# Kernel optimization log

Measured on AMD Instinct MI355X. Metric: run time of the kernel, lower is better.

Reference implementation:

```python
import jax, jax.numpy as jnp
import numpy as np
import math

B, L, E, H, K = 4, 1024, 1024, 16, 64
D = E // H  # head_dim = 64; rel_pe has 2K+1 = 129 rows


def setup_inputs() -> dict:
    key = jax.random.key(0)
    ks = jax.random.split(key, 4)
    s = 1.0 / math.sqrt(E)
    return {
        "q": jax.random.normal(ks[0], (B, L, E), dtype=jnp.float32),
        "in_proj_weight": jax.random.normal(ks[1], (3 * E, E), dtype=jnp.float32) * s,
        "in_proj_bias": jnp.zeros((3 * E,), dtype=jnp.float32),
        "out_w": jax.random.normal(ks[2], (E, E), dtype=jnp.float32) * s,
        "out_b": jnp.zeros((E,), dtype=jnp.float32),
        "rel_pe": jax.random.normal(ks[3], (2 * K + 1, D), dtype=jnp.float32) * (1.0 / math.sqrt(D)),
    }


def _attend(q, in_proj_weight, in_proj_bias, out_w, out_b, rel_pe):
    b, l, e = q.shape
    h, d = H, D
    qkv = q @ in_proj_weight.T + in_proj_bias  # (B, L, 3E)
    qh, kh, vh = jnp.split(qkv, 3, axis=-1)
    # (B, L, E) -> (B, H, L, D)
    qh = qh.reshape(b, l, h, d).transpose(0, 2, 1, 3)
    kh = kh.reshape(b, l, h, d).transpose(0, 2, 1, 3)
    vh = vh.reshape(b, l, h, d).transpose(0, 2, 1, 3)
    qh = qh / math.sqrt(d)  # scaling applies to both content and position terms
    # content scores
    scores = jnp.einsum("bhid,bhjd->bhij", qh, kh)
    # relative-position bias: a[i, j] = rel_pe[clip(j - i, -K, K) + K]
    # compute q . rel_pe once, then gather per (i, j) -- same math as the
    # original O(L^2 * D) materialized tensor, without building it.
    pos = jnp.arange(l)
    rel = jnp.clip(pos[None, :] - pos[:, None], -K, K) + K  # (L, L) int
    bias_r = jnp.einsum("bhid,rd->bhir", qh, rel_pe)  # (B, H, L, 2K+1)
    bias = jnp.take_along_axis(bias_r, jnp.broadcast_to(rel[None, None], (b, h, l, l)), axis=-1)
    attn = jax.nn.softmax(scores + bias, axis=-1)
    out = jnp.einsum("bhij,bhjd->bhid", attn, vh)  # (B, H, L, D)
    out = out.transpose(0, 2, 1, 3).reshape(b, l, e)
    return out @ out_w.T + out_b


def reference(q, in_proj_weight, in_proj_bias, out_w, out_b, rel_pe):
    return _attend(q, in_proj_weight, in_proj_bias, out_w, out_b, rel_pe)
```

## Files before the change

### kernel.cpp

```cpp
#include <hip/hip_runtime.h>
#include <math.h>

typedef _Float16 half_t;
typedef _Float16 half8 __attribute__((ext_vector_type(8)));
typedef _Float16 half4v __attribute__((ext_vector_type(4)));
typedef float float4v __attribute__((ext_vector_type(4)));
typedef float float16v __attribute__((ext_vector_type(16)));

#define AS1 __attribute__((address_space(1)))
#define AS3 __attribute__((address_space(3)))

#define MFMA16(a, b, c) __builtin_amdgcn_mfma_f32_16x16x32_f16((a), (b), (c), 0, 0, 0)
#define MFMA32(a, b, c) __builtin_amdgcn_mfma_f32_32x32x16_f16((a), (b), (c), 0, 0, 0)

__device__ __forceinline__ void gload16(const half_t* g, half_t* l) {
    __builtin_amdgcn_global_load_lds((const AS1 void*)g, (AS3 void*)l, 16, 0, 0);
}

__device__ __forceinline__ int iclamp(int v, int lo, int hi) {
    return v < lo ? lo : (v > hi ? hi : v);
}

__global__ __launch_bounds__(256) void cast_kernel(
    const float* __restrict__ q, const float* __restrict__ w_in,
    const float* __restrict__ w_out, const float* __restrict__ pe,
    half_t* __restrict__ q16, half_t* __restrict__ w16,
    half_t* __restrict__ wo16, half_t* __restrict__ pe16)
{
    const int tid = blockIdx.x * 256 + threadIdx.x;
    const int stride = gridDim.x * 256;
    for (int i = tid; i < 1048576; i += stride) {
        float4 v = ((const float4*)q)[i];
        *(half4v*)(q16 + (size_t)i * 4) =
            (half4v){(half_t)v.x, (half_t)v.y, (half_t)v.z, (half_t)v.w};
    }
    for (int i = tid; i < 786432; i += stride) {
        float4 v = ((const float4*)w_in)[i];
        *(half4v*)(w16 + (size_t)i * 4) =
            (half4v){(half_t)v.x, (half_t)v.y, (half_t)v.z, (half_t)v.w};
    }
    for (int i = tid; i < 262144; i += stride) {
        float4 v = ((const float4*)w_out)[i];
        *(half4v*)(wo16 + (size_t)i * 4) =
            (half4v){(half_t)v.x, (half_t)v.y, (half_t)v.z, (half_t)v.w};
    }
    for (int i = tid; i < 2064; i += stride) {
        float4 v = ((const float4*)pe)[i];
        *(half4v*)(pe16 + (size_t)i * 4) =
            (half4v){(half_t)v.x, (half_t)v.y, (half_t)v.z, (half_t)v.w};
    }
    for (int i = tid; i < 496; i += stride) {
        *(half4v*)(pe16 + 8256 + (size_t)i * 4) = (half4v){0, 0, 0, 0};
    }
}

__global__ __launch_bounds__(256) void qkv_gemm(
    const half_t* __restrict__ A, const half_t* __restrict__ W,
    const float* __restrict__ bias,
    half_t* __restrict__ qh, half_t* __restrict__ kh, half_t* __restrict__ vt)
{
    __shared__ half_t As[128 * 32];
    __shared__ half_t Bs[128 * 32];
    const int K = 1024;
    const int tid = threadIdx.x, lane = tid & 63, wid = tid >> 6;
    const int wm = wid & 1, wn = wid >> 1;
    const int bid = blockIdx.x;
    const int xcd = bid & 7, idx = bid >> 3;
    const int m0 = (((xcd >> 1) << 3) + (idx & 7)) * 128;
    const int n0 = (((xcd & 1) * 12) + (idx >> 3)) * 128;

    const half_t* gA[2]; const half_t* gB[2];
    half_t* lA[2]; half_t* lB[2];
    {
        const int base = wid * 128;
#pragma unroll
        for (int c = 0; c < 2; ++c) {
            int slot = base + c * 64 + lane;
            int row = slot >> 2;
            int ch = (slot & 3) ^ ((row >> 1) & 3);
            gA[c] = A + (size_t)(m0 + row) * K + ch * 8;
            gB[c] = W + (size_t)(n0 + row) * K + ch * 8;
            lA[c] = As + (base + c * 64) * 8;
            lB[c] = Bs + (base + c * 64) * 8;
        }
    }
    int aOff[4], bOff[4];
#pragma unroll
    for (int i = 0; i < 4; ++i) {
        int ra = wm * 64 + i * 16 + (lane & 15);
        aOff[i] = ra * 32 + (((lane >> 4) ^ ((ra >> 1) & 3)) * 8);
        int rb = wn * 64 + i * 16 + (lane & 15);
        bOff[i] = rb * 32 + (((lane >> 4) ^ ((rb >> 1) & 3)) * 8);
    }
    float4v acc[4][4];
#pragma unroll
    for (int i = 0; i < 4; ++i)
#pragma unroll
        for (int j = 0; j < 4; ++j) acc[i][j] = (float4v){0.f, 0.f, 0.f, 0.f};

    for (int k0 = 0; k0 < K; k0 += 32) {
        __syncthreads();
        gload16(gA[0], lA[0]); gload16(gA[1], lA[1]);
        gload16(gB[0], lB[0]); gload16(gB[1], lB[1]);
        gA[0] += 32; gA[1] += 32; gB[0] += 32; gB[1] += 32;
        __syncthreads();
        half8 af[4], bf[4];
#pragma unroll
        for (int i = 0; i < 4; ++i) af[i] = *(const half8*)(As + aOff[i]);
#pragma unroll
        for (int j = 0; j < 4; ++j) bf[j] = *(const half8*)(Bs + bOff[j]);
#pragma unroll
        for (int i = 0; i < 4; ++i)
#pragma unroll
            for (int j = 0; j < 4; ++j)
                acc[i][j] = MFMA16(af[i], bf[j], acc[i][j]);
    }

    const int part = n0 >> 10;
#pragma unroll
    for (int ni = 0; ni < 4; ++ni) {
        const int col = n0 + wn * 64 + ni * 16 + (lane & 15);
        const float bv = bias[col];
        const int hh = (col >> 6) & 15, d = col & 63;
#pragma unroll
        for (int mi = 0; mi < 4; ++mi) {
            const int r0 = m0 + wm * 64 + mi * 16 + ((lane >> 4) << 2);
            const int bb = r0 >> 10, l0 = r0 & 1023;
            if (part == 0) {
#pragma unroll
                for (int r = 0; r < 4; ++r)
                    qh[(((size_t)(bb * 16 + hh) * 1024) + l0 + r) * 64 + d] =
                        (half_t)((acc[mi][ni][r] + bv) * 0.125f);
            } else if (part == 1) {
#pragma unroll
                for (int r = 0; r < 4; ++r)
                    kh[(((size_t)(bb * 16 + hh) * 1024) + l0 + r) * 64 + d] =
                        (half_t)(acc[mi][ni][r] + bv);
            } else {
                half4v pk;
#pragma unroll
                for (int r = 0; r < 4; ++r) pk[r] = (half_t)(acc[mi][ni][r] + bv);
                *(half4v*)(vt + ((size_t)(bb * 16 + hh) * 64 + d) * 1024 + l0) = pk;
            }
        }
    }
}

__global__ __launch_bounds__(256) void out_gemm(
    const half_t* __restrict__ A, const half_t* __restrict__ W,
    const float* __restrict__ bias, float* __restrict__ C)
{
    __shared__ half_t As[128 * 32];
    __shared__ half_t Bs[64 * 32];
    const int K = 1024;
    const int tid = threadIdx.x, lane = tid & 63, wid = tid >> 6;
    const int wm = wid & 1, wn = wid >> 1;
    const int bid = blockIdx.x;
    const int xcd = bid & 7, idx = bid >> 3;
    const int m0 = ((xcd << 2) + (idx >> 4)) * 128;
    const int n0 = (idx & 15) * 64;

    const half_t* gA[2]; const half_t* gB1;
    half_t* lA[2]; half_t* lB1;
    {
        const int base = wid * 128;
#pragma unroll
        for (int c = 0; c < 2; ++c) {
            int slot = base + c * 64 + lane;
            int row = slot >> 2;
            int ch = (slot & 3) ^ ((row >> 1) & 3);
            gA[c] = A + (size_t)(m0 + row) * K + ch * 8;
            lA[c] = As + (base + c * 64) * 8;
        }
        int slotB = wid * 64 + lane;
        int rowB = slotB >> 2;
        int chB = (slotB & 3) ^ ((rowB >> 1) & 3);
        gB1 = W + (size_t)(n0 + rowB) * K + chB * 8;
        lB1 = Bs + (wid * 64) * 8;
    }
    int aOff[4], bOff[2];
#pragma unroll
    for (int i = 0; i < 4; ++i) {
        int ra = wm * 64 + i * 16 + (lane & 15);
        aOff[i] = ra * 32 + (((lane >> 4) ^ ((ra >> 1) & 3)) * 8);
    }
#pragma unroll
    for (int j = 0; j < 2; ++j) {
        int rb = wn * 32 + j * 16 + (lane & 15);
        bOff[j] = rb * 32 + (((lane >> 4) ^ ((rb >> 1) & 3)) * 8);
    }
    float4v acc[4][2];
#pragma unroll
    for (int i = 0; i < 4; ++i)
#pragma unroll
        for (int j = 0; j < 2; ++j) acc[i][j] = (float4v){0.f, 0.f, 0.f, 0.f};

    for (int k0 = 0; k0 < K; k0 += 32) {
        __syncthreads();
        gload16(gA[0], lA[0]); gload16(gA[1], lA[1]);
        gload16(gB1, lB1);
        gA[0] += 32; gA[1] += 32; gB1 += 32;
        __syncthreads();
        half8 af[4], bf[2];
#pragma unroll
        for (int i = 0; i < 4; ++i) af[i] = *(const half8*)(As + aOff[i]);
#pragma unroll
        for (int j = 0; j < 2; ++j) bf[j] = *(const half8*)(Bs + bOff[j]);
#pragma unroll
        for (int i = 0; i < 4; ++i)
#pragma unroll
            for (int j = 0; j < 2; ++j)
                acc[i][j] = MFMA16(af[i], bf[j], acc[i][j]);
    }

#pragma unroll
    for (int ni = 0; ni < 2; ++ni) {
        const int col = n0 + wn * 32 + ni * 16 + (lane & 15);
        const float bv = bias[col];
#pragma unroll
        for (int mi = 0; mi < 4; ++mi) {
            const int r0 = m0 + wm * 64 + mi * 16 + ((lane >> 4) << 2);
#pragma unroll
            for (int r = 0; r < 4; ++r)
                C[(size_t)(r0 + r) * 1024 + col] = acc[mi][ni][r] + bv;
        }
    }
}

__global__ __launch_bounds__(256) void attn_mfma(
    const half_t* __restrict__ qh, const half_t* __restrict__ kh,
    const half_t* __restrict__ vt, const half_t* __restrict__ pe,
    half_t* __restrict__ ao)
{
    __shared__ half_t KV[8192];
    __shared__ half_t Pm[4 * 2048];
    __shared__ half_t R2[4 * 32 * 172];

    const int tid = threadIdx.x, lane = tid & 63, wid = tid >> 6;
    const int hl = lane >> 5, ql = lane & 31;
    const int bid = blockIdx.x;
    const int xcd = bid & 7, idx = bid >> 3;
    const int bh = xcd + ((idx >> 3) << 3);
    const int q0 = (idx & 7) * 128;
    const int h = bh & 15, b = bh >> 4;
    const int i0w = q0 + wid * 32;
    const size_t hbase = (size_t)(b * 16 + h) * 64 * 1024;
    const half_t* Qg = qh + hbase;
    const half_t* Kg = kh + hbase;
    const half_t* Vg = vt + hbase;

    const int qrow = i0w + ql;
    half8 qb[4];
#pragma unroll
    for (int cc = 0; cc < 4; ++cc)
        qb[cc] = *(const half8*)(Qg + (size_t)qrow * 64 + cc * 16 + hl * 8);

    const half_t* gS[4]; int lOff[4]; int ginc[4];
#pragma unroll
    for (int c = 0; c < 4; ++c) {
        const int slot0 = wid * 256 + c * 64;
        const int slot = slot0 + lane;
        if (slot0 < 512) {
            int srow = slot >> 3, sch = (slot & 7) ^ (srow & 7);
            gS[c] = Kg + srow * 64 + sch * 8;
            ginc[c] = 64 * 64;
            lOff[c] = slot0 * 8;
        } else {
            int s2 = slot - 512;
            int srow = s2 >> 3, sch = (s2 & 7) ^ (srow & 7);
            gS[c] = Vg + srow * 1024 + sch * 8;
            ginc[c] = 64;
            lOff[c] = 4096 + (slot0 - 512) * 8;
        }
    }

    half_t* r2w = R2 + wid * (32 * 172);
#pragma unroll
    for (int j2 = 0; j2 < 5; ++j2) {
        float16v c;
#pragma unroll
        for (int r = 0; r < 16; ++r) c[r] = 0.f;
#pragma unroll
        for (int cc = 0; cc < 4; ++cc) {
            half8 pb = *(const half8*)(pe + (size_t)(j2 * 32 + ql) * 64 + cc * 16 + hl * 8);
            c = MFMA32(qb[cc], pb, c);
        }
        const int col = j2 * 32 + ql;
        if (col < 129) {
#pragma unroll
            for (int reg = 0; reg < 16; ++reg) {
                const int il = (reg & 3) + 8 * (reg >> 2) + 4 * hl;
                const half_t hv = (half_t)(c[reg] - 2.0f);
                if (col == 0) {
                    for (int ts = 0; ts <= il + 4; ++ts) r2w[il * 172 + ts] = hv;
                } else if (col == 128) {
                    for (int ts = il + 132; ts <= il + 139; ++ts) r2w[il * 172 + ts] = hv;
                } else {
                    r2w[il * 172 + col + 4 + il] = hv;
                }
            }
        }
    }

    int kOff[2][4], vOff[2][4], pOff[4];
#pragma unroll
    for (int t2 = 0; t2 < 2; ++t2)
#pragma unroll
        for (int cc = 0; cc < 4; ++cc) {
            int row = t2 * 32 + ql;
            int ch = (cc * 2 + hl) ^ (row & 7);
            kOff[t2][cc] = row * 64 + ch * 8;
            vOff[t2][cc] = 4096 + row * 64 + ch * 8;
        }
    const int pwSw = (ql & 7) * 8;
    const int pwBase = wid * 2048 + ql * 64;
#pragma unroll
    for (int cc = 0; cc < 4; ++cc)
        pOff[cc] = pwBase + ((cc * 16 + hl * 8) ^ pwSw);

    const int hiC = 128 + ((ql + 3) & ~3);
    const half_t* r2row = r2w + ql * 172;

    float l_r = 0.f;
    float16v oacc[2];
#pragma unroll
    for (int dt = 0; dt < 2; ++dt)
#pragma unroll
        for (int r = 0; r < 16; ++r) oacc[dt][r] = 0.f;

    for (int kt = 0; kt < 16; ++kt) {
        __syncthreads();
#pragma unroll
        for (int c = 0; c < 4; ++c) { gload16(gS[c], KV + lOff[c]); gS[c] += ginc[c]; }
        __syncthreads();

#pragma unroll
        for (int t2 = 0; t2 < 2; ++t2) {
            float16v s;
#pragma unroll
            for (int g = 0; g < 4; ++g) {
                int traw = kt * 64 + t2 * 32 + 8 * g + 4 * hl + 64 - i0w;
                int tsb = iclamp(traw, -4, hiC) + 4;
                half4v bh4 = *(const half4v*)(r2row + tsb);
#pragma unroll
                for (int r = 0; r < 4; ++r) s[4 * g + r] = (float)bh4[r];
            }
#pragma unroll
            for (int cc = 0; cc < 4; ++cc) {
                half8 kf = *(const half8*)(KV + kOff[t2][cc]);
                s = MFMA32(kf, qb[cc], s);
            }
#pragma unroll
            for (int g = 0; g < 4; ++g) {
                half4v ph;
#pragma unroll
                for (int r = 0; r < 4; ++r) {
                    float p = __expf(s[4 * g + r]);
                    l_r += p;
                    ph[r] = (half_t)p;
                }
                const int kvb = t2 * 32 + 8 * g + 4 * hl;
                *(half4v*)(Pm + pwBase + (kvb ^ pwSw)) = ph;
            }
        }

        half8 pf[4];
#pragma unroll
        for (int cc = 0; cc < 4; ++cc) pf[cc] = *(const half8*)(Pm + pOff[cc]);
#pragma unroll
        for (int dt = 0; dt < 2; ++dt)
#pragma unroll
            for (int cc = 0; cc < 4; ++cc) {
                half8 vf = *(const half8*)(KV + vOff[dt][cc]);
                oacc[dt] = MFMA32(vf, pf[cc], oacc[dt]);
            }
    }

    l_r += __shfl_xor(l_r, 32);
    const float inv = 1.0f / l_r;

    half_t* aorow = ao + ((size_t)(b * 1024 + i0w + ql)) * 1024 + h * 64;
#pragma unroll
    for (int dt = 0; dt < 2; ++dt)
#pragma unroll
        for (int g = 0; g < 4; ++g) {
            const int d0 = dt * 32 + 8 * g + 4 * hl;
            half4v oh;
#pragma unroll
            for (int r = 0; r < 4; ++r) oh[r] = (half_t)(oacc[dt][4 * g + r] * inv);
            *(half4v*)(aorow + d0) = oh;
        }
}

extern "C" void kernel_launch(void* const* d_in, const int* in_sizes, int n_in,
                              void* d_out, int out_size, void* d_ws, size_t ws_size,
                              hipStream_t stream) {
    const float* q     = (const float*)d_in[0];
    const float* w_in  = (const float*)d_in[1];
    const float* b_in  = (const float*)d_in[2];
    const float* w_out = (const float*)d_in[3];
    const float* b_out = (const float*)d_in[4];
    const float* pe    = (const float*)d_in[5];
    float* out = (float*)d_out;

    half_t* ws = (half_t*)d_ws;
    half_t* q16   = ws;
    half_t* w16   = q16 + 4194304;
    half_t* wo16  = w16 + 3145728;
    half_t* pe16  = wo16 + 1048576;
    half_t* qh16  = pe16 + 10240;
    half_t* kh16  = qh16 + 4194304;
    half_t* vt16  = kh16 + 4194304;
    half_t* ao16  = vt16 + 4194304;

    cast_kernel<<<2048, 256, 0, stream>>>(q, w_in, w_out, pe, q16, w16, wo16, pe16);
    qkv_gemm<<<768, 256, 0, stream>>>(q16, w16, b_in, qh16, kh16, vt16);
    attn_mfma<<<512, 256, 0, stream>>>(qh16, kh16, vt16, pe16, ao16);
    out_gemm<<<512, 256, 0, stream>>>(ao16, wo16, b_out, out);
}
```

Measured before the change: 181.0 us.

## Double-buffer K/V tiles, use exp2 with folded log2e, keep P in registers

Double-buffers the K/V LDS tiles so the global-to-LDS load of the next tile overlaps compute on the current one, replacing the two per-iteration syncthreads with waitcnt plus a barrier. The softmax scale and fixed offset are premultiplied by log2(e) so the raw exp2 instruction replaces __expf. The P matrix is now passed from the QK MFMA output layout to the PV operand layout with permlane32_swap instead of a round-trip through LDS. This frees the LDS used for P but doubles the KV buffer, and the hand-written waitcnt sequencing is fragile.

```diff
diff --git a/kernel.cpp b/kernel.cpp
--- a/kernel.cpp
+++ b/kernel.cpp
@@ -12,6 +12,9 @@
 
 #define MFMA16(a, b, c) __builtin_amdgcn_mfma_f32_16x16x32_f16((a), (b), (c), 0, 0, 0)
 #define MFMA32(a, b, c) __builtin_amdgcn_mfma_f32_32x32x16_f16((a), (b), (c), 0, 0, 0)
+
+#define QSCALE 0.18033688f
+#define TABOFF 2.88539008f
 
 __device__ __forceinline__ void gload16(const half_t* g, half_t* l) {
     __builtin_amdgcn_global_load_lds((const AS1 void*)g, (AS3 void*)l, 16, 0, 0);
@@ -130,7 +133,7 @@
 #pragma unroll
                 for (int r = 0; r < 4; ++r)
                     qh[(((size_t)(bb * 16 + hh) * 1024) + l0 + r) * 64 + d] =
-                        (half_t)((acc[mi][ni][r] + bv) * 0.125f);
+                        (half_t)((acc[mi][ni][r] + bv) * QSCALE);
             } else if (part == 1) {
 #pragma unroll
                 for (int r = 0; r < 4; ++r)
@@ -232,8 +235,7 @@
     const half_t* __restrict__ vt, const half_t* __restrict__ pe,
     half_t* __restrict__ ao)
 {
-    __shared__ half_t KV[8192];
-    __shared__ half_t Pm[4 * 2048];
+    __shared__ half_t KV[2 * 8192];
     __shared__ half_t R2[4 * 32 * 172];
 
     const int tid = threadIdx.x, lane = tid & 63, wid = tid >> 6;
@@ -248,12 +250,6 @@
     const half_t* Qg = qh + hbase;
     const half_t* Kg = kh + hbase;
     const half_t* Vg = vt + hbase;
-
-    const int qrow = i0w + ql;
-    half8 qb[4];
-#pragma unroll
-    for (int cc = 0; cc < 4; ++cc)
-        qb[cc] = *(const half8*)(Qg + (size_t)qrow * 64 + cc * 16 + hl * 8);
 
     const half_t* gS[4]; int lOff[4]; int ginc[4];
 #pragma unroll
@@ -274,6 +270,15 @@
         }
     }
 
+#pragma unroll
+    for (int c = 0; c < 4; ++c) { gload16(gS[c], KV + lOff[c]); gS[c] += ginc[c]; }
+
+    const int qrow = i0w + ql;
+    half8 qb[4];
+#pragma unroll
+    for (int cc = 0; cc < 4; ++cc)
+        qb[cc] = *(const half8*)(Qg + (size_t)qrow * 64 + cc * 16 + hl * 8);
+
     half_t* r2w = R2 + wid * (32 * 172);
 #pragma unroll
     for (int j2 = 0; j2 < 5; ++j2) {
@@ -290,7 +295,7 @@
 #pragma unroll
             for (int reg = 0; reg < 16; ++reg) {
                 const int il = (reg & 3) + 8 * (reg >> 2) + 4 * hl;
-                const half_t hv = (half_t)(c[reg] - 2.0f);
+                const half_t hv = (half_t)(c[reg] - TABOFF);
                 if (col == 0) {
                     for (int ts = 0; ts <= il + 4; ++ts) r2w[il * 172 + ts] = hv;
                 } else if (col == 128) {
@@ -301,8 +306,9 @@
             }
         }
     }
-
-    int kOff[2][4], vOff[2][4], pOff[4];
+    asm volatile("s_waitcnt lgkmcnt(0)" ::: "memory");
+
+    int kOff[2][4], vOff[2][4];
 #pragma unroll
     for (int t2 = 0; t2 < 2; ++t2)
 #pragma unroll
@@ -312,11 +318,6 @@
             kOff[t2][cc] = row * 64 + ch * 8;
             vOff[t2][cc] = 4096 + row * 64 + ch * 8;
         }
-    const int pwSw = (ql & 7) * 8;
-    const int pwBase = wid * 2048 + ql * 64;
-#pragma unroll
-    for (int cc = 0; cc < 4; ++cc)
-        pOff[cc] = pwBase + ((cc * 16 + hl * 8) ^ pwSw);
 
     const int hiC = 128 + ((ql + 3) & ~3);
     const half_t* r2row = r2w + ql * 172;
@@ -328,52 +329,78 @@
 #pragma unroll
         for (int r = 0; r < 16; ++r) oacc[dt][r] = 0.f;
 
-    for (int kt = 0; kt < 16; ++kt) {
-        __syncthreads();
-#pragma unroll
-        for (int c = 0; c < 4; ++c) { gload16(gS[c], KV + lOff[c]); gS[c] += ginc[c]; }
-        __syncthreads();
-
-#pragma unroll
-        for (int t2 = 0; t2 < 2; ++t2) {
-            float16v s;
-#pragma unroll
-            for (int g = 0; g < 4; ++g) {
-                int traw = kt * 64 + t2 * 32 + 8 * g + 4 * hl + 64 - i0w;
-                int tsb = iclamp(traw, -4, hiC) + 4;
-                half4v bh4 = *(const half4v*)(r2row + tsb);
-#pragma unroll
-                for (int r = 0; r < 4; ++r) s[4 * g + r] = (float)bh4[r];
+    for (int kt2 = 0; kt2 < 8; ++kt2) {
+#pragma unroll
+        for (int kk = 0; kk < 2; ++kk) {
+            const int kt = kt2 * 2 + kk;
+            if (kt < 15) {
+#pragma unroll
+                for (int c = 0; c < 4; ++c) {
+                    gload16(gS[c], KV + (kk ^ 1) * 8192 + lOff[c]);
+                    gS[c] += ginc[c];
+                }
+                asm volatile("s_waitcnt vmcnt(4)" ::: "memory");
+            } else {
+                asm volatile("s_waitcnt vmcnt(0)" ::: "memory");
             }
+            __builtin_amdgcn_s_barrier();
+            asm volatile("" ::: "memory");
+
+            const half_t* KVb = KV + kk * 8192;
+
+            half4v preg[2][4];
+#pragma unroll
+            for (int t2 = 0; t2 < 2; ++t2) {
+                float16v s;
+#pragma unroll
+                for (int g = 0; g < 4; ++g) {
+                    int traw = kt * 64 + t2 * 32 + 8 * g + 4 * hl + 64 - i0w;
+                    int tsb = iclamp(traw, -4, hiC) + 4;
+                    half4v bh4 = *(const half4v*)(r2row + tsb);
+#pragma unroll
+                    for (int r = 0; r < 4; ++r) s[4 * g + r] = (float)bh4[r];
+                }
+#pragma unroll
+                for (int cc = 0; cc < 4; ++cc) {
+                    half8 kf = *(const half8*)(KVb + kOff[t2][cc]);
+                    s = MFMA32(kf, qb[cc], s);
+                }
+#pragma unroll
+                for (int g = 0; g < 4; ++g) {
+#pragma unroll
+                    for (int r = 0; r < 4; ++r) {
+                        float p = __builtin_amdgcn_exp2f(s[4 * g + r]);
+                        l_r += p;
+                        preg[t2][g][r] = (half_t)p;
+                    }
+                }
+            }
+
+            half8 pf[4];
 #pragma unroll
             for (int cc = 0; cc < 4; ++cc) {
-                half8 kf = *(const half8*)(KV + kOff[t2][cc]);
-                s = MFMA32(kf, qb[cc], s);
+                half4v pA = preg[cc >> 1][(cc & 1) * 2];
+                half4v pB = preg[cc >> 1][(cc & 1) * 2 + 1];
+                unsigned ad[2], bd[2];
+                __builtin_memcpy(ad, &pA, 8);
+                __builtin_memcpy(bd, &pB, 8);
+                auto r0 = __builtin_amdgcn_permlane32_swap(ad[0], bd[0], false, false);
+                auto r1 = __builtin_amdgcn_permlane32_swap(ad[1], bd[1], false, false);
+                unsigned pfw[4] = {r0[0], r1[0], r0[1], r1[1]};
+                __builtin_memcpy(&pf[cc], pfw, 16);
             }
-#pragma unroll
-            for (int g = 0; g < 4; ++g) {
-                half4v ph;
-#pragma unroll
-                for (int r = 0; r < 4; ++r) {
-                    float p = __expf(s[4 * g + r]);
-                    l_r += p;
-                    ph[r] = (half_t)p;
-                }
-                const int kvb = t2 * 32 + 8 * g + 4 * hl;
-                *(half4v*)(Pm + pwBase + (kvb ^ pwSw)) = ph;
-            }
-        }
-
-        half8 pf[4];
-#pragma unroll
-        for (int cc = 0; cc < 4; ++cc) pf[cc] = *(const half8*)(Pm + pOff[cc]);
-#pragma unroll
-        for (int dt = 0; dt < 2; ++dt)
-#pragma unroll
-            for (int cc = 0; cc < 4; ++cc) {
-                half8 vf = *(const half8*)(KV + vOff[dt][cc]);
-                oacc[dt] = MFMA32(vf, pf[cc], oacc[dt]);
-            }
+
+#pragma unroll
+            for (int dt = 0; dt < 2; ++dt)
+#pragma unroll
+                for (int cc = 0; cc < 4; ++cc) {
+                    half8 vf = *(const half8*)(KVb + vOff[dt][cc]);
+                    oacc[dt] = MFMA32(vf, pf[cc], oacc[dt]);
+                }
+
+            asm volatile("" ::: "memory");
+            __builtin_amdgcn_s_barrier();
+        }
     }
 
     l_r += __shfl_xor(l_r, 32);
```

Measured after the change: 177.8 us. Within noise of the previous version (-1.8%).
